# Optimization experiments

Hardware: AMD Instinct MI355X
Metric: run time of the kernel (lower is better)

## Reference

```python
import jax, jax.numpy as jnp
import numpy as np

# Static config (Swin-T stage 1, SW-MSA)
B = 32; H = 56; W = 56; C = 96; NH = 3; WS = 7; SHIFT = 3
N = WS * WS                 # tokens per window (49)
NW = (H // WS) * (W // WS)  # windows per image (64)
HD = C // NH                # head dim (32)
SCALE = HD ** -0.5
EPS = 1e-3  # keras LayerNormalization default epsilon


def _rel_index():
    # Matches tf.stack(tf.meshgrid(h, w)) with default 'xy' indexing
    xx, yy = np.meshgrid(np.arange(WS), np.arange(WS))
    coords = np.stack([xx, yy]).reshape(2, -1)              # [2, 49]
    rel = (coords[:, :, None] - coords[:, None, :]).transpose(1, 2, 0)
    rel[:, :, 0] += WS - 1
    rel[:, :, 1] += WS - 1
    rel[:, :, 0] *= 2 * WS - 1
    return rel.sum(-1)                                       # [49, 49]

REL_IDX = jnp.asarray(_rel_index())


def _attn_mask():
    # Standard Swin shifted-window attention mask
    img = np.zeros((H, W))
    cnt = 0
    sl = (slice(0, -WS), slice(-WS, -SHIFT), slice(-SHIFT, None))
    for hs in sl:
        for ws_ in sl:
            img[hs, ws_] = cnt
            cnt += 1
    win = img.reshape(H // WS, WS, W // WS, WS).transpose(0, 2, 1, 3).reshape(-1, N)
    diff = win[:, None, :] - win[:, :, None]
    return jnp.asarray(np.where(diff != 0, -100.0, 0.0), dtype=np.float32)  # [nW,49,49]

MASK = _attn_mask()


def _ln(x, g, b):
    mu = x.mean(-1, keepdims=True)
    var = ((x - mu) ** 2).mean(-1, keepdims=True)
    return (x - mu) / jnp.sqrt(var + EPS) * g + b


def setup_inputs() -> dict:
    key = jax.random.key(0)
    ks = jax.random.split(key, 6)
    f32 = jnp.float32
    return {
        "x": jax.random.normal(ks[0], (B, H * W, C), f32),
        "norm1_g": jnp.ones((C,), f32), "norm1_b": jnp.zeros((C,), f32),
        "qkv_w": jax.random.normal(ks[1], (C, 3 * C), f32) * 0.02,
        "qkv_b": jnp.zeros((3 * C,), f32),
        "bias_table": jax.random.normal(ks[2], ((2 * WS - 1) ** 2, NH), f32) * 0.02,
        "proj_w": jax.random.normal(ks[3], (C, C), f32) * 0.02,
        "proj_b": jnp.zeros((C,), f32),
        "norm2_g": jnp.ones((C,), f32), "norm2_b": jnp.zeros((C,), f32),
        "fc1_w": jax.random.normal(ks[4], (C, 4 * C), f32) * 0.02,
        "fc1_b": jnp.zeros((4 * C,), f32),
        "fc2_w": jax.random.normal(ks[5], (4 * C, C), f32) * 0.02,
        "fc2_b": jnp.zeros((C,), f32),
    }


def reference(x, norm1_g, norm1_b, qkv_w, qkv_b, bias_table, proj_w, proj_b,
              norm2_g, norm2_b, fc1_w, fc1_b, fc2_w, fc2_b):
    shortcut = x
    h = _ln(x, norm1_g, norm1_b).reshape(B, H, W, C)
    # cyclic shift (SW-MSA)
    h = jnp.roll(h, (-SHIFT, -SHIFT), axis=(1, 2))
    # window partition -> [B*nW, N, C]
    h = h.reshape(B, H // WS, WS, W // WS, WS, C).transpose(0, 1, 3, 2, 4, 5).reshape(-1, N, C)
    qkv = (h @ qkv_w + qkv_b).reshape(-1, N, 3, NH, HD).transpose(2, 0, 3, 1, 4)
    q, k, v = qkv[0], qkv[1], qkv[2]            # each [B*nW, NH, N, HD]
    attn = jnp.einsum('bhnd,bhmd->bhnm', q * SCALE, k)
    bias = bias_table[REL_IDX.reshape(-1)].reshape(N, N, NH).transpose(2, 0, 1)
    attn = attn + bias[None]
    attn = attn.reshape(B, NW, NH, N, N) + MASK[None, :, None]
    attn = attn.reshape(-1, NH, N, N)
    # NOTE: source applies softmax twice (once in branch, once unconditionally)
    attn = jax.nn.softmax(jax.nn.softmax(attn, axis=-1), axis=-1)
    o = jnp.einsum('bhnm,bhmd->bhnd', attn, v).transpose(0, 2, 1, 3).reshape(-1, N, C)
    o = o @ proj_w + proj_b
    # window reverse + reverse cyclic shift
    o = o.reshape(B, H // WS, W // WS, WS, WS, C).transpose(0, 1, 3, 2, 4, 5).reshape(B, H, W, C)
    o = jnp.roll(o, (SHIFT, SHIFT), axis=(1, 2)).reshape(B, H * W, C)
    x = shortcut + o
    y = _ln(x, norm2_g, norm2_b)
    # NOTE: source Mlp applies gelu in Dense activation AND again in call -> double gelu
    y = jax.nn.gelu(y @ fc1_w + fc1_b, approximate=False)
    y = jax.nn.gelu(y, approximate=False)
    y = y @ fc2_w + fc2_b
    return x + y
```

## Files before the change

kernel.cpp:

```cpp
#include <hip/hip_runtime.h>
#include <math.h>

#define BB   32
#define HH   56
#define WWI  56
#define CC   96
#define NHD  3
#define WSZ  7
#define SHF  3
#define NTK  49
#define NWIN 64
#define HDM  32
#define TOT  (BB*HH*WWI)
#define QKSCALE 0.17677669529663687f
#define LEPS 1e-3f

typedef __attribute__((ext_vector_type(8))) short s8v;
typedef __attribute__((ext_vector_type(4))) float fx4;
typedef unsigned long long ull_t;

#define MFMA16(a,b,c) __builtin_amdgcn_mfma_f32_16x16x32_bf16((a),(b),(c),0,0,0)

__device__ __forceinline__ unsigned short f2bf(float f) {
    union { float f; unsigned u; } v; v.f = f;
    unsigned r = v.u + 0x7FFFu + ((v.u >> 16) & 1u);
    return (unsigned short)(r >> 16);
}

__device__ __forceinline__ float gelu_t(float x) {
    float x3 = x * x * x;
    float z = -1.5957691216f * fmaf(0.044715f, x3, x);
    return x * __builtin_amdgcn_rcpf(1.f + __expf(z));
}

__device__ __forceinline__ int wtok_to_orig(int wt) {
    int win = wt / NTK;
    int p   = wt - win * NTK;
    int b   = win >> 6;
    int w   = win & 63;
    int wi = w >> 3, wj = w & 7;
    int pi = p / WSZ, pj = p - pi * WSZ;
    int r = wi * WSZ + pi + SHF; if (r >= HH) r -= HH;
    int c = wj * WSZ + pj + SHF; if (c >= WWI) c -= WWI;
    return b * (HH * WWI) + r * WWI + c;
}

__device__ __forceinline__ void ln_frag(const float* __restrict__ row,
                                        const float* __restrict__ gg,
                                        const float* __restrict__ bb,
                                        int g4, s8v ha[3])
{
    float h[24];
    #pragma unroll
    for (int ks = 0; ks < 3; ++ks) {
        fx4 v0 = *reinterpret_cast<const fx4*>(row + ks * 32 + g4 * 8);
        fx4 v1 = *reinterpret_cast<const fx4*>(row + ks * 32 + g4 * 8 + 4);
        h[ks*8+0]=v0.x; h[ks*8+1]=v0.y; h[ks*8+2]=v0.z; h[ks*8+3]=v0.w;
        h[ks*8+4]=v1.x; h[ks*8+5]=v1.y; h[ks*8+6]=v1.z; h[ks*8+7]=v1.w;
    }
    float s = 0.f, s2 = 0.f;
    #pragma unroll
    for (int j = 0; j < 24; ++j) { s += h[j]; s2 = fmaf(h[j], h[j], s2); }
    s  += __shfl_xor(s, 16);  s  += __shfl_xor(s, 32);
    s2 += __shfl_xor(s2, 16); s2 += __shfl_xor(s2, 32);
    const float mu = s * (1.f/CC);
    const float rs = rsqrtf(s2 * (1.f/CC) - mu * mu + LEPS);
    #pragma unroll
    for (int ks = 0; ks < 3; ++ks) {
        union { s8v v; unsigned short u[8]; } p;
        #pragma unroll
        for (int j = 0; j < 8; ++j) {
            int c = ks * 32 + g4 * 8 + j;
            p.u[j] = f2bf((h[ks*8+j] - mu) * rs * gg[c] + bb[c]);
        }
        ha[ks] = p.v;
    }
}

extern "C" __global__ void p0_prep(const float* __restrict__ qw, const float* __restrict__ pw,
                                   const float* __restrict__ w1, const float* __restrict__ w2,
                                   const float* __restrict__ btab,
                                   unsigned short* __restrict__ wsw)
{
    int i = blockIdx.x * 256 + threadIdx.x;
    if (i < 27648) {
        int e = i & 7, f = i >> 3;
        int lane = f & 63, fid = f >> 6;
        int ks = fid % 3, t = fid / 3;
        int nt = t % 6, ck = t / 6;
        int n = ck * 96 + nt * 16 + (lane & 15);
        int k = ks * 32 + (lane >> 4) * 8 + e;
        float v = qw[k * 288 + n];
        if (n < 96) v *= QKSCALE;
        wsw[i] = f2bf(v);
    } else if (i < 36864) {
        int j = i - 27648;
        int e = j & 7, f = j >> 3;
        int lane = f & 63, fid = f >> 6;
        int ks = fid % 3, nt = fid / 3;
        int n = nt * 16 + (lane & 15);
        int k = ks * 32 + (lane >> 4) * 8 + e;
        wsw[i] = f2bf(pw[k * 96 + n]);
    } else if (i < 73728) {
        int j = i - 36864;
        int e = j & 7, f = j >> 3;
        int lane = f & 63, fid = f >> 6;
        int ks = fid % 3, t = fid / 3;
        int nt = t & 3, ck = t >> 2;
        int n = ck * 64 + nt * 16 + (lane & 15);
        int k = ks * 32 + (lane >> 4) * 8 + e;
        wsw[i] = f2bf(w1[k * 384 + n]);
    } else if (i < 110592) {
        int j = i - 73728;
        int e = j & 7, f = j >> 3;
        int lane = f & 63, fid = f >> 6;
        int ks = fid & 1, t = fid >> 1;
        int nt = t % 6, ck = t / 6;
        int n = nt * 16 + (lane & 15);
        int k = ck * 64 + ks * 32 + (lane >> 4) * 8 + e;
        wsw[i] = f2bf(w2[k * 96 + n]);
    } else if (i < 148224) {
        float* bm = (float*)(wsw + 110592);
        int j = i - 110592;
        int n = j & 63, mh = j >> 6;
        int m = mh % 49, t = mh / 49;
        int hd = t % 3, cls = t / 3;
        float val = 0.f;
        if (n < 49) {
            int it = m / 7, jt = m - it * 7;
            int iu = n / 7, ju = n - iu * 7;
            int li  = (cls & 2) ? (it < 4 ? 1 : 2) : 0;
            int lj  = (cls & 1) ? (jt < 4 ? 1 : 2) : 0;
            int lui = (cls & 2) ? (iu < 4 ? 1 : 2) : 0;
            int luj = (cls & 1) ? (ju < 4 ? 1 : 2) : 0;
            int bidx = (jt - ju + 6) * 13 + (it - iu + 6);
            val = btab[bidx * 3 + hd] + ((li*3+lj) == (lui*3+luj) ? 0.f : -100.f);
        }
        bm[j] = val;
    }
}

extern "C" __global__ void __launch_bounds__(256, 3) k1_qkv(
    const float* __restrict__ x, const float* __restrict__ g1, const float* __restrict__ b1,
    const unsigned short* __restrict__ qwtf, const float* __restrict__ qb,
    unsigned short* __restrict__ qkvb)
{
    const int tid = threadIdx.x, wave = tid >> 6, lane = tid & 63;
    const int l15 = lane & 15, g4 = lane >> 4;
    const int row0 = blockIdx.x * 64 + wave * 16;

    s8v ha[3];
    {
        const int orig = wtok_to_orig(row0 + l15);
        ln_frag(x + (size_t)orig * CC, g1, b1, g4, ha);
    }

    #pragma unroll
    for (int ck = 0; ck < 3; ++ck) {
        fx4 acc[6];
        #pragma unroll
        for (int nt = 0; nt < 6; ++nt) acc[nt] = (fx4){0.f,0.f,0.f,0.f};
        #pragma unroll
        for (int ks = 0; ks < 3; ++ks) {
            #pragma unroll
            for (int nt = 0; nt < 6; ++nt) {
                s8v b = *reinterpret_cast<const s8v*>(
                    &qwtf[(((ck * 6 + nt) * 3 + ks) * 64 + lane) * 8]);
                acc[nt] = MFMA16(ha[ks], b, acc[nt]);
            }
        }
        const int rowb = row0 + g4 * 4;
        const float qmul = (ck == 0) ? QKSCALE : 1.f;
        #pragma unroll
        for (int nt = 0; nt < 6; ++nt) {
            const int col = ck * 96 + nt * 16 + l15;
            const float qbc = qb[col] * qmul;
            #pragma unroll
            for (int r = 0; r < 4; ++r)
                qkvb[(size_t)(rowb + r) * 288 + col] = f2bf(acc[nt][r] + qbc);
        }
    }
}

extern "C" __global__ void __launch_bounds__(64, 2) k2_attn(
    unsigned short* __restrict__ qkvb, const float* __restrict__ bm)
{
    __shared__ unsigned short P[64][72];
    const int lane = threadIdx.x;
    const int l15 = lane & 15, g4 = lane >> 4;
    const int task = blockIdx.x;
    const int win = task / 3, h = task - win * 3;
    const int g0  = win * NTK;
    const int w   = win & 63;
    const int cls = (((w >> 3) == 7) ? 2 : 0) + (((w & 7) == 7) ? 1 : 0);
    const float* BMh = bm + ((size_t)(cls * 3 + h)) * 49 * 64;

    s8v aq[4], bk[4];
    #pragma unroll
    for (int mt = 0; mt < 4; ++mt) {
        int tok = mt * 16 + l15; if (tok > 48) tok = 48;
        const unsigned short* qp = &qkvb[(size_t)(g0 + tok) * 288 + h * HDM + g4 * 8];
        aq[mt] = *reinterpret_cast<const s8v*>(qp);
        bk[mt] = *reinterpret_cast<const s8v*>(qp + 96);
    }

    fx4 sc[4][4];
    #pragma unroll
    for (int mt = 0; mt < 4; ++mt)
        #pragma unroll
        for (int nt = 0; nt < 4; ++nt)
            sc[mt][nt] = MFMA16(aq[mt], bk[nt], ((fx4){0.f,0.f,0.f,0.f}));

    #pragma unroll
    for (int mt = 0; mt < 4; ++mt) {
        #pragma unroll
        for (int r = 0; r < 4; ++r) {
            const int m = mt * 16 + g4 * 4 + r;
            const int mc = m > 48 ? 48 : m;
            float rs1 = 0.f;
            #pragma unroll
            for (int nt = 0; nt < 4; ++nt) {
                const int n = nt * 16 + l15;
                float s = sc[mt][nt][r] + BMh[mc * 64 + n];
                float e = (n < NTK) ? __expf(s) : 0.f;
                sc[mt][nt][r] = e;
                rs1 += e;
            }
            rs1 += __shfl_xor(rs1, 1); rs1 += __shfl_xor(rs1, 2);
            rs1 += __shfl_xor(rs1, 4); rs1 += __shfl_xor(rs1, 8);
            const float iv1 = 1.f / rs1;
            float rs2 = 0.f;
            #pragma unroll
            for (int nt = 0; nt < 4; ++nt) {
                const int n = nt * 16 + l15;
                float e2 = (n < NTK) ? __expf(sc[mt][nt][r] * iv1) : 0.f;
                sc[mt][nt][r] = e2;
                rs2 += e2;
            }
            rs2 += __shfl_xor(rs2, 1); rs2 += __shfl_xor(rs2, 2);
            rs2 += __shfl_xor(rs2, 4); rs2 += __shfl_xor(rs2, 8);
            const float iv2 = 1.f / rs2;
            #pragma unroll
            for (int nt = 0; nt < 4; ++nt)
                P[m][nt * 16 + l15] = f2bf(sc[mt][nt][r] * iv2);
        }
    }
    __syncthreads();

    fx4 oc[4][2];
    #pragma unroll
    for (int mt = 0; mt < 4; ++mt) { oc[mt][0] = (fx4){0.f,0.f,0.f,0.f}; oc[mt][1] = (fx4){0.f,0.f,0.f,0.f}; }
    #pragma unroll
    for (int ks = 0; ks < 2; ++ks) {
        s8v vb[2];
        #pragma unroll
        for (int nt = 0; nt < 2; ++nt) {
            union { s8v v; unsigned short u[8]; } pv;
            #pragma unroll
            for (int j = 0; j < 8; ++j) {
                int tok = ks * 32 + g4 * 8 + j; if (tok > 48) tok = 48;
                pv.u[j] = qkvb[(size_t)(g0 + tok) * 288 + 192 + h * HDM + nt * 16 + l15];
            }
            vb[nt] = pv.v;
        }
        #pragma unroll
        for (int mt = 0; mt < 4; ++mt) {
            s8v pa = *reinterpret_cast<const s8v*>(&P[mt * 16 + l15][ks * 32 + g4 * 8]);
            oc[mt][0] = MFMA16(pa, vb[0], oc[mt][0]);
            oc[mt][1] = MFMA16(pa, vb[1], oc[mt][1]);
        }
    }
    #pragma unroll
    for (int mt = 0; mt < 4; ++mt) {
        #pragma unroll
        for (int r = 0; r < 4; ++r) {
            const int m = mt * 16 + g4 * 4 + r;
            if (m < NTK) {
                qkvb[(size_t)(g0 + m) * 288 + h * HDM + l15]      = f2bf(oc[mt][0][r]);
                qkvb[(size_t)(g0 + m) * 288 + h * HDM + 16 + l15] = f2bf(oc[mt][1][r]);
            }
        }
    }
}

extern "C" __global__ void __launch_bounds__(256, 3) k2b_proj(
    const unsigned short* __restrict__ qkvb, const unsigned short* __restrict__ pwtf,
    const float* __restrict__ pb, const float* __restrict__ x, float* __restrict__ out)
{
    const int tid = threadIdx.x, wave = tid >> 6, lane = tid & 63;
    const int l15 = lane & 15, g4 = lane >> 4;
    const int row0 = blockIdx.x * 64 + wave * 16;

    const unsigned short* arow = qkvb + (size_t)(row0 + l15) * 288 + g4 * 8;
    s8v a[3];
    a[0] = *reinterpret_cast<const s8v*>(arow);
    a[1] = *reinterpret_cast<const s8v*>(arow + 32);
    a[2] = *reinterpret_cast<const s8v*>(arow + 64);

    fx4 acc[6];
    #pragma unroll
    for (int nt = 0; nt < 6; ++nt) acc[nt] = (fx4){0.f,0.f,0.f,0.f};
    #pragma unroll
    for (int ks = 0; ks < 3; ++ks) {
        #pragma unroll
        for (int nt = 0; nt < 6; ++nt) {
            s8v b = *reinterpret_cast<const s8v*>(&pwtf[((nt * 3 + ks) * 64 + lane) * 8]);
            acc[nt] = MFMA16(a[ks], b, acc[nt]);
        }
    }
    int orig[4];
    #pragma unroll
    for (int r = 0; r < 4; ++r)
        orig[r] = wtok_to_orig(row0 + g4 * 4 + r);
    #pragma unroll
    for (int nt = 0; nt < 6; ++nt) {
        const int col = nt * 16 + l15;
        const float pbc = pb[col];
        #pragma unroll
        for (int r = 0; r < 4; ++r) {
            const size_t idx = (size_t)orig[r] * CC + col;
            out[idx] = acc[nt][r] + pbc + x[idx];
        }
    }
}

#define LDA 72
extern "C" __global__ void __launch_bounds__(256, 3) k3_mlp(
    float* __restrict__ xio, const float* __restrict__ g2, const float* __restrict__ b2,
    const unsigned short* __restrict__ w1f, const float* __restrict__ bf1,
    const unsigned short* __restrict__ w2f, const float* __restrict__ bf2)
{
    __shared__ unsigned short Ac[64 * LDA];
    const int tid = threadIdx.x, wave = tid >> 6, lane = tid & 63;
    const int l15 = lane & 15, g4 = lane >> 4;
    const int row0 = blockIdx.x * 64 + wave * 16;

    s8v ha[3];
    ln_frag(xio + (size_t)(row0 + l15) * CC, g2, b2, g4, ha);

    fx4 oacc[6];
    #pragma unroll
    for (int nt = 0; nt < 6; ++nt) oacc[nt] = (fx4){0.f,0.f,0.f,0.f};

    #pragma unroll
    for (int ck = 0; ck < 6; ++ck) {
        fx4 a1[4];
        #pragma unroll
        for (int nt = 0; nt < 4; ++nt) a1[nt] = (fx4){0.f,0.f,0.f,0.f};
        #pragma unroll
        for (int ks = 0; ks < 3; ++ks) {
            #pragma unroll
            for (int nt = 0; nt < 4; ++nt) {
                s8v b = *reinterpret_cast<const s8v*>(
                    &w1f[(((ck * 4 + nt) * 3 + ks) * 64 + lane) * 8]);
                a1[nt] = MFMA16(ha[ks], b, a1[nt]);
            }
        }
        #pragma unroll
        for (int nt = 0; nt < 4; ++nt) {
            const float bb = bf1[ck * 64 + nt * 16 + l15];
            #pragma unroll
            for (int r = 0; r < 4; ++r) {
                float v0 = a1[nt][r] + bb;
                Ac[(wave*16 + g4*4 + r) * LDA + nt*16 + l15] = f2bf(gelu_t(gelu_t(v0)));
            }
        }
        #pragma unroll
        for (int ks = 0; ks < 2; ++ks) {
            s8v a = *reinterpret_cast<const s8v*>(&Ac[(wave*16 + l15)*LDA + ks*32 + g4*8]);
            #pragma unroll
            for (int nt = 0; nt < 6; ++nt) {
                s8v b = *reinterpret_cast<const s8v*>(
                    &w2f[(((ck * 6 + nt) * 2 + ks) * 64 + lane) * 8]);
                oacc[nt] = MFMA16(a, b, oacc[nt]);
            }
        }
    }

    const int rowb = row0 + g4 * 4;
    #pragma unroll
    for (int nt = 0; nt < 6; ++nt) {
        const int col = nt * 16 + l15;
        const float bb = bf2[col];
        #pragma unroll
        for (int r = 0; r < 4; ++r) {
            const size_t idx = (size_t)(rowb + r) * CC + col;
            xio[idx] = xio[idx] + oacc[nt][r] + bb;
        }
    }
}

extern "C" void kernel_launch(void* const* d_in, const int* in_sizes, int n_in,
                              void* d_out, int out_size, void* d_ws, size_t ws_size,
                              hipStream_t stream)
{
    const float* x    = (const float*)d_in[0];
    const float* n1g  = (const float*)d_in[1];
    const float* n1b  = (const float*)d_in[2];
    const float* qw   = (const float*)d_in[3];
    const float* qb   = (const float*)d_in[4];
    const float* btab = (const float*)d_in[5];
    const float* pw   = (const float*)d_in[6];
    const float* pb   = (const float*)d_in[7];
    const float* n2g  = (const float*)d_in[8];
    const float* n2b  = (const float*)d_in[9];
    const float* w1   = (const float*)d_in[10];
    const float* bf1  = (const float*)d_in[11];
    const float* w2   = (const float*)d_in[12];
    const float* bf2  = (const float*)d_in[13];
    float* out = (float*)d_out;

    unsigned short* qkvb = (unsigned short*)d_ws;
    unsigned short* wbf  = qkvb + (size_t)TOT * 288;
    unsigned short* qwtf = wbf;
    unsigned short* pwtf = qwtf + 27648;
    unsigned short* w1f  = pwtf + 9216;
    unsigned short* w2f  = w1f + 36864;
    float* bmt = (float*)(wbf + 110592);

    p0_prep <<<579, 256, 0, stream>>>(qw, pw, w1, w2, btab, wbf);
    k1_qkv  <<<TOT/64, 256, 0, stream>>>(x, n1g, n1b, qwtf, qb, qkvb);
    k2_attn <<<BB*NWIN*NHD, 64, 0, stream>>>(qkvb, bmt);
    k2b_proj<<<TOT/64, 256, 0, stream>>>(qkvb, pwtf, pb, x, out);
    k3_mlp  <<<TOT/64, 256, 0, stream>>>(out, n2g, n2b, w1f, bf1, w2f, bf2);
}
```

Before: 148.9 us.

## Store V and bias-mask tables in MFMA fragment order for attention kernel

```diff
diff --git a/kernel.cpp b/kernel.cpp
--- a/kernel.cpp
+++ b/kernel.cpp
@@ -119,12 +119,16 @@
         int n = nt * 16 + (lane & 15);
         int k = ck * 64 + ks * 32 + (lane >> 4) * 8 + e;
         wsw[i] = f2bf(w2[k * 96 + n]);
-    } else if (i < 148224) {
-        float* bm = (float*)(wsw + 110592);
+    } else if (i < 159744) {
+        float* bmf = (float*)(wsw + 110592);
         int j = i - 110592;
-        int n = j & 63, mh = j >> 6;
-        int m = mh % 49, t = mh / 49;
+        int r = j & 3, lane = (j >> 2) & 63;
+        int fid = j >> 8;
+        int mtnt = fid & 15, t = fid >> 4;
+        int mt = mtnt >> 2, nt = mtnt & 3;
         int hd = t % 3, cls = t / 3;
+        int m = mt * 16 + (lane >> 4) * 4 + r; if (m > 48) m = 48;
+        int n = nt * 16 + (lane & 15);
         float val = 0.f;
         if (n < 49) {
             int it = m / 7, jt = m - it * 7;
@@ -136,14 +140,14 @@
             int bidx = (jt - ju + 6) * 13 + (it - iu + 6);
             val = btab[bidx * 3 + hd] + ((li*3+lj) == (lui*3+luj) ? 0.f : -100.f);
         }
-        bm[j] = val;
+        bmf[j] = val;
     }
 }
 
 extern "C" __global__ void __launch_bounds__(256, 3) k1_qkv(
     const float* __restrict__ x, const float* __restrict__ g1, const float* __restrict__ b1,
     const unsigned short* __restrict__ qwtf, const float* __restrict__ qb,
-    unsigned short* __restrict__ qkvb)
+    unsigned short* __restrict__ qkvb, unsigned short* __restrict__ vF)
 {
     const int tid = threadIdx.x, wave = tid >> 6, lane = tid & 63;
     const int l15 = lane & 15, g4 = lane >> 4;
@@ -170,20 +174,40 @@
             }
         }
         const int rowb = row0 + g4 * 4;
-        const float qmul = (ck == 0) ? QKSCALE : 1.f;
-        #pragma unroll
-        for (int nt = 0; nt < 6; ++nt) {
-            const int col = ck * 96 + nt * 16 + l15;
-            const float qbc = qb[col] * qmul;
-            #pragma unroll
-            for (int r = 0; r < 4; ++r)
-                qkvb[(size_t)(rowb + r) * 288 + col] = f2bf(acc[nt][r] + qbc);
+        if (ck < 2) {
+            const float qmul = (ck == 0) ? QKSCALE : 1.f;
+            #pragma unroll
+            for (int nt = 0; nt < 6; ++nt) {
+                const int col = ck * 96 + nt * 16 + l15;
+                const float qbc = qb[col] * qmul;
+                #pragma unroll
+                for (int r = 0; r < 4; ++r)
+                    qkvb[(size_t)(rowb + r) * 288 + col] = f2bf(acc[nt][r] + qbc);
+            }
+        } else {
+            #pragma unroll
+            for (int nt = 0; nt < 6; ++nt) {
+                const int dg  = nt * 16 + l15;
+                const float qbc = qb[192 + dg];
+                const int hh  = dg >> 5, dd = dg & 31;
+                const int ntp = dd >> 4, llo = dd & 15;
+                #pragma unroll
+                for (int r = 0; r < 4; ++r) {
+                    const int tok = rowb + r;
+                    const int win = tok / 49, p = tok - win * 49;
+                    const int ksp = p >> 5, rem = p & 31;
+                    const int g4p = rem >> 3, jj = rem & 7;
+                    vF[((size_t)(win * 3 + hh) * 4 + ksp * 2 + ntp) * 512 +
+                       (g4p * 16 + llo) * 8 + jj] = f2bf(acc[nt][r] + qbc);
+                }
+            }
         }
     }
 }
 
 extern "C" __global__ void __launch_bounds__(64, 2) k2_attn(
-    unsigned short* __restrict__ qkvb, const float* __restrict__ bm)
+    unsigned short* __restrict__ qkvb, const unsigned short* __restrict__ vF,
+    const float* __restrict__ bmf)
 {
     __shared__ unsigned short P[64][72];
     const int lane = threadIdx.x;
@@ -193,7 +217,8 @@
     const int g0  = win * NTK;
     const int w   = win & 63;
     const int cls = (((w >> 3) == 7) ? 2 : 0) + (((w & 7) == 7) ? 1 : 0);
-    const float* BMh = bm + ((size_t)(cls * 3 + h)) * 49 * 64;
+    const float* BMF = bmf + (size_t)(cls * 3 + h) * 4096;
+    const unsigned short* vFwh = vF + (size_t)(win * 3 + h) * 2048;
 
     s8v aq[4], bk[4];
     #pragma unroll
@@ -213,15 +238,17 @@
 
     #pragma unroll
     for (int mt = 0; mt < 4; ++mt) {
+        fx4 bmv[4];
+        #pragma unroll
+        for (int nt = 0; nt < 4; ++nt)
+            bmv[nt] = *reinterpret_cast<const fx4*>(&BMF[((mt * 4 + nt) << 8) + lane * 4]);
         #pragma unroll
         for (int r = 0; r < 4; ++r) {
-            const int m = mt * 16 + g4 * 4 + r;
-            const int mc = m > 48 ? 48 : m;
             float rs1 = 0.f;
             #pragma unroll
             for (int nt = 0; nt < 4; ++nt) {
                 const int n = nt * 16 + l15;
-                float s = sc[mt][nt][r] + BMh[mc * 64 + n];
+                float s = sc[mt][nt][r] + bmv[nt][r];
                 float e = (n < NTK) ? __expf(s) : 0.f;
                 sc[mt][nt][r] = e;
                 rs1 += e;
@@ -240,6 +267,7 @@
             rs2 += __shfl_xor(rs2, 1); rs2 += __shfl_xor(rs2, 2);
             rs2 += __shfl_xor(rs2, 4); rs2 += __shfl_xor(rs2, 8);
             const float iv2 = 1.f / rs2;
+            const int m = mt * 16 + g4 * 4 + r;
             #pragma unroll
             for (int nt = 0; nt < 4; ++nt)
                 P[m][nt * 16 + l15] = f2bf(sc[mt][nt][r] * iv2);
@@ -254,15 +282,8 @@
     for (int ks = 0; ks < 2; ++ks) {
         s8v vb[2];
         #pragma unroll
-        for (int nt = 0; nt < 2; ++nt) {
-            union { s8v v; unsigned short u[8]; } pv;
-            #pragma unroll
-            for (int j = 0; j < 8; ++j) {
-                int tok = ks * 32 + g4 * 8 + j; if (tok > 48) tok = 48;
-                pv.u[j] = qkvb[(size_t)(g0 + tok) * 288 + 192 + h * HDM + nt * 16 + l15];
-            }
-            vb[nt] = pv.v;
-        }
+        for (int nt = 0; nt < 2; ++nt)
+            vb[nt] = *reinterpret_cast<const s8v*>(&vFwh[((ks * 2 + nt) * 64 + lane) * 8]);
         #pragma unroll
         for (int mt = 0; mt < 4; ++mt) {
             s8v pa = *reinterpret_cast<const s8v*>(&P[mt * 16 + l15][ks * 32 + g4 * 8]);
@@ -342,7 +363,7 @@
     #pragma unroll
     for (int nt = 0; nt < 6; ++nt) oacc[nt] = (fx4){0.f,0.f,0.f,0.f};
 
-    #pragma unroll
+    #pragma unroll 1
     for (int ck = 0; ck < 6; ++ck) {
         fx4 a1[4];
         #pragma unroll
@@ -416,11 +437,12 @@
     unsigned short* pwtf = qwtf + 27648;
     unsigned short* w1f  = pwtf + 9216;
     unsigned short* w2f  = w1f + 36864;
-    float* bmt = (float*)(wbf + 110592);
-
-    p0_prep <<<579, 256, 0, stream>>>(qw, pw, w1, w2, btab, wbf);
-    k1_qkv  <<<TOT/64, 256, 0, stream>>>(x, n1g, n1b, qwtf, qb, qkvb);
-    k2_attn <<<BB*NWIN*NHD, 64, 0, stream>>>(qkvb, bmt);
+    float* bmf = (float*)(wbf + 110592);
+    unsigned short* vF = wbf + 110592 + 98304;
+
+    p0_prep <<<624, 256, 0, stream>>>(qw, pw, w1, w2, btab, wbf);
+    k1_qkv  <<<TOT/64, 256, 0, stream>>>(x, n1g, n1b, qwtf, qb, qkvb, vF);
+    k2_attn <<<BB*NWIN*NHD, 64, 0, stream>>>(qkvb, vF, bmf);
     k2b_proj<<<TOT/64, 256, 0, stream>>>(qkvb, pwtf, pb, x, out);
     k3_mlp  <<<TOT/64, 256, 0, stream>>>(out, n2g, n2b, w1f, bf1, w2f, bf2);
 }
```

Measured after the change: 144.7 us. 1.03x faster.
